# Kernel optimization log

Hardware: AMD Instinct MI355X
Metric: run time of the kernel (lower is better)

The kernel has to match this reference:

```python
import jax, jax.numpy as jnp
import numpy as np

N_EMB = 1024
N_HEADS = 16
HS = N_EMB // N_HEADS  # 64
BASE = 10000.0


def _rope_cache(T):
    # theta uses dim = n_emb (as in the source), sliced to hs//2 frequencies
    i = jnp.arange(HS // 2, dtype=jnp.float32)
    theta = BASE ** (-2.0 * i / N_EMB)            # [hs/2]
    pos = jnp.arange(T, dtype=jnp.float32)        # [T]
    ang = pos[:, None] * theta[None, :]           # [T, hs/2]
    return jnp.cos(ang), jnp.sin(ang)


def _apply_rope(x, cos, sin):
    # x: [B, T, nh, hs]; rotate consecutive pairs along hs
    b, t, nh, hs = x.shape
    xr = x.reshape(b, t, nh, hs // 2, 2)
    c = cos[None, :, None, :]
    s = sin[None, :, None, :]
    r0 = xr[..., 0] * c - xr[..., 1] * s
    r1 = xr[..., 1] * c + xr[..., 0] * s
    return jnp.stack([r0, r1], axis=-1).reshape(b, t, nh, hs)


def setup_inputs() -> dict:
    key = jax.random.key(0)
    k1, k2, k3, k4 = jax.random.split(key, 4)
    B, T = 2, 2048
    w_std = 0.02
    x = jax.random.normal(k1, (B, T, N_EMB), jnp.float32)
    Wq = jax.random.normal(k2, (N_EMB, N_EMB), jnp.float32) * w_std
    Wk = jax.random.normal(k3, (N_EMB, N_EMB), jnp.float32) * w_std
    Wv = jax.random.normal(k4, (N_EMB, N_EMB), jnp.float32) * w_std
    return {"x": x, "Wq": Wq, "Wk": Wk, "Wv": Wv}


def reference(x, Wq, Wk, Wv):
    B, T, C = x.shape
    # nn.Linear(bias=False): y = x @ W.T
    q = (x @ Wq.T).reshape(B, T, N_HEADS, HS)
    k = (x @ Wk.T).reshape(B, T, N_HEADS, HS)
    v = (x @ Wv.T).reshape(B, T, N_HEADS, HS)
    cos, sin = _rope_cache(T)
    q = _apply_rope(q, cos, sin)
    k = _apply_rope(k, cos, sin)
    # scale uses C (n_emb), as in the source (not head_size)
    wei = jnp.einsum('bqhd,bkhd->bhqk', q, k) * (C ** -0.5)  # [B, nh, T, T]
    mask = jnp.tril(jnp.ones((T, T), dtype=bool))
    wei = jnp.where(mask[None, None], wei, -jnp.inf)
    wei = jax.nn.softmax(wei, axis=-1)
    # dropout is identity in eval mode
    out = jnp.einsum('bhqk,bkhd->bqhd', wei, v).reshape(B, T, C)
    return out
```

## Files before the change

kernel.cpp:

```cpp
#include <hip/hip_runtime.h>
#include <stdint.h>

typedef unsigned short u16;
typedef __bf16 bf16x8 __attribute__((ext_vector_type(8)));
typedef unsigned short u16x8 __attribute__((ext_vector_type(8)));
typedef float f32x4 __attribute__((ext_vector_type(4)));

#define LOG2E 1.4426950408889634f

typedef const __attribute__((address_space(1))) uint32_t as1_u32;
typedef __attribute__((address_space(3))) uint32_t as3_u32;

__device__ __forceinline__ u16 f2bf(float f) {
  union { float f; uint32_t i; } v; v.f = f;
  uint32_t r = (v.i + 0x7fffu + ((v.i >> 16) & 1u)) >> 16;
  return (u16)r;
}
__device__ __forceinline__ float bf2f(u16 u) {
  union { uint32_t i; float f; } v; v.i = ((uint32_t)u) << 16; return v.f;
}

__device__ __forceinline__ void gld_lds16(const void* g, void* l) {
  as1_u32* gp = (as1_u32*)((uintptr_t)g);
  as3_u32* lp = (as3_u32*)(uint32_t)(uintptr_t)(l);
  __builtin_amdgcn_global_load_lds(gp, lp, 16, 0, 0);
}

__global__ __launch_bounds__(256) void f32_to_bf16(
    const float* __restrict__ x, const float* __restrict__ wq,
    const float* __restrict__ wk, const float* __restrict__ wv,
    u16* __restrict__ xc, u16* __restrict__ wqc,
    u16* __restrict__ wkc, u16* __restrict__ wvc) {
  const int z = blockIdx.y;
  const float* src = z == 0 ? x : (z == 1 ? wq : (z == 2 ? wk : wv));
  u16* dst = z == 0 ? xc : (z == 1 ? wqc : (z == 2 ? wkc : wvc));
  const int n = z == 0 ? (1 << 22) : (1 << 20);

  const int idx = (blockIdx.x * 256 + (int)threadIdx.x) * 8;
  if (idx >= n) return;
  const f32x4 a = *(const f32x4*)&src[idx];
  const f32x4 b = *(const f32x4*)&src[idx + 4];
  u16x8 o;
#pragma unroll
  for (int j = 0; j < 4; j++) { o[j] = f2bf(a[j]); o[j + 4] = f2bf(b[j]); }
  *(u16x8*)&dst[idx] = o;
}

__global__ __launch_bounds__(256) void qkv_gemm(
    const u16* __restrict__ xc, const u16* __restrict__ wqc,
    const u16* __restrict__ wkc, const u16* __restrict__ wvc,
    u16* __restrict__ qo, u16* __restrict__ ko, u16* __restrict__ vt) {
  __shared__ __align__(16) u16 As[128 * 32];
  __shared__ __align__(16) u16 Bs[128 * 32];

  const int tid = threadIdx.x;
  const int lane = tid & 63;
  const int w = tid >> 6;
  const int wm = w >> 1, wn = w & 1;
  const int quad = lane >> 4, m16 = lane & 15;
  const int which = blockIdx.z;

  const u16* __restrict__ Ap;
  const u16* __restrict__ Bp;
  int m0, n0;
  if (which == 2) {
    Ap = wvc; Bp = xc;
    m0 = blockIdx.x * 128;
    n0 = blockIdx.y * 128;
  } else {
    Ap = xc; Bp = which == 0 ? wqc : wkc;
    m0 = blockIdx.y * 128;
    n0 = blockIdx.x * 128;
  }

  const f32x4 z4 = {0.f, 0.f, 0.f, 0.f};
  f32x4 acc[4][4];
#pragma unroll
  for (int i = 0; i < 4; i++)
#pragma unroll
    for (int j = 0; j < 4; j++) acc[i][j] = z4;

  const int rowA = m0 + w * 32 + (lane >> 2);
  const int rowB = n0 + w * 32 + (lane >> 2);
  const int cch = (lane & 3) * 8;

  for (int k0 = 0; k0 < 1024; k0 += 32) {
    __syncthreads();
#pragma unroll
    for (int i = 0; i < 2; i++) {
      gld_lds16(&Ap[(size_t)(rowA + i * 16) * 1024 + k0 + cch],
                &As[(w * 32 + i * 16) * 32]);
      gld_lds16(&Bp[(size_t)(rowB + i * 16) * 1024 + k0 + cch],
                &Bs[(w * 32 + i * 16) * 32]);
    }
    __syncthreads();

    bf16x8 af[4], bfr[4];
#pragma unroll
    for (int t = 0; t < 4; t++) {
      af[t]  = *(const bf16x8*)&As[(wm * 64 + t * 16 + m16) * 32 + quad * 8];
      bfr[t] = *(const bf16x8*)&Bs[(wn * 64 + t * 16 + m16) * 32 + quad * 8];
    }
#pragma unroll
    for (int mt = 0; mt < 4; mt++)
#pragma unroll
      for (int nt = 0; nt < 4; nt++)
        acc[mt][nt] = __builtin_amdgcn_mfma_f32_16x16x32_bf16(
            af[mt], bfr[nt], acc[mt][nt], 0, 0, 0);
  }

  if (which < 2) {
    u16* __restrict__ out = which == 0 ? qo : ko;
#pragma unroll
    for (int mt = 0; mt < 4; mt++) {
      const int row = m0 + wm * 64 + mt * 16 + quad * 4;
#pragma unroll
      for (int nt = 0; nt < 4; nt++) {
        const int n = n0 + wn * 64 + nt * 16 + m16;
        f32x4 a = acc[mt][nt];
#pragma unroll
        for (int r = 0; r < 4; r++)
          out[(size_t)(row + r) * 1024 + n] = f2bf(a[r]);
      }
    }
  } else {
#pragma unroll
    for (int mt = 0; mt < 4; mt++) {
      const int row = m0 + wm * 64 + mt * 16 + quad * 4;
#pragma unroll
      for (int nt = 0; nt < 4; nt++) {
        const int n = n0 + wn * 64 + nt * 16 + m16;
        f32x4 a = acc[mt][nt];
#pragma unroll
        for (int r = 0; r < 4; r++)
          vt[(size_t)(row + r) * 4096 + n] = f2bf(a[r]);
      }
    }
  }
}

__global__ __launch_bounds__(256) void rope_inplace(u16* __restrict__ qb,
                                                    u16* __restrict__ kb) {
  u16* buf = blockIdx.y == 0 ? qb : kb;
  const int p = blockIdx.x * 256 + (int)threadIdx.x;
  const int nidx = p * 2;
  const int row = nidx >> 10;
  const int col = nidx & 1023;
  const int i = (col & 63) >> 1;
  const int t = row & 2047;
  const float theta = exp2f(-(float)i * 0.02595256324130752f);
  const float ang = (float)t * theta;
  float s, c;
  sincosf(ang, &s, &c);
  const float a0 = bf2f(buf[(size_t)row * 1024 + col]);
  const float a1 = bf2f(buf[(size_t)row * 1024 + col + 1]);
  buf[(size_t)row * 1024 + col]     = f2bf(a0 * c - a1 * s);
  buf[(size_t)row * 1024 + col + 1] = f2bf(a1 * c + a0 * s);
}

__global__ __launch_bounds__(256) void flash_attn(
    const u16* __restrict__ qg, const u16* __restrict__ kg,
    const u16* __restrict__ vt, float* __restrict__ out) {
  __shared__ __align__(16) u16 Qs[64 * 72];
  __shared__ __align__(16) u16 Ks[64 * 72];
  __shared__ __align__(16) u16 Vs[64 * 72];
  __shared__ __align__(16) u16 Ps[64 * 72];

  const int tid = threadIdx.x, lane = tid & 63, w = tid >> 6;
  const int quad = lane >> 4, m16 = lane & 15;
  const int h = blockIdx.y, b = blockIdx.z;
  const size_t base = (size_t)b * 2048 * 1024 + (size_t)h * 64;
  const size_t vbase = (size_t)(h * 64) * 4096 + (size_t)b * 2048;
  const float SC = 0.03125f * LOG2E;

  const f32x4 z4 = {0.f, 0.f, 0.f, 0.f};
  const int srow = tid >> 2, sc = (tid & 3) * 16;

  for (int pass = 0; pass < 2; ++pass) {
    const int qt = pass == 0 ? (int)blockIdx.x : 31 - (int)blockIdx.x;
    const int q0 = qt * 64;

    __syncthreads();
    {
      const u16* src = &qg[base + (size_t)(q0 + srow) * 1024 + sc];
      *(u16x8*)&Qs[srow * 72 + sc] = *(const u16x8*)src;
      *(u16x8*)&Qs[srow * 72 + sc + 8] = *(const u16x8*)(src + 8);
    }
    u16x8 kr0, kr1, vr0, vr1;
    {
      const u16* ks = &kg[base + (size_t)srow * 1024 + sc];
      kr0 = *(const u16x8*)ks; kr1 = *(const u16x8*)(ks + 8);
      const u16* vs = &vt[vbase + (size_t)srow * 4096 + sc];
      vr0 = *(const u16x8*)vs; vr1 = *(const u16x8*)(vs + 8);
    }
    __syncthreads();
    const bf16x8 qf0 = *(const bf16x8*)&Qs[(w * 16 + m16) * 72 + quad * 8];
    const bf16x8 qf1 = *(const bf16x8*)&Qs[(w * 16 + m16) * 72 + 32 + quad * 8];

    float l_p[4] = {0.f, 0.f, 0.f, 0.f};
    f32x4 O[4];
#pragma unroll
    for (int d = 0; d < 4; d++) O[d] = z4;

    const int qrow0 = q0 + w * 16 + quad * 4;

    for (int kt = 0; kt <= qt; ++kt) {
      const int k0 = kt * 64;
      if (kt) __syncthreads();
      *(u16x8*)&Ks[srow * 72 + sc] = kr0;
      *(u16x8*)&Ks[srow * 72 + sc + 8] = kr1;
      *(u16x8*)&Vs[srow * 72 + sc] = vr0;
      *(u16x8*)&Vs[srow * 72 + sc + 8] = vr1;
      __syncthreads();
      if (kt < qt) {
        const u16* ks = &kg[base + (size_t)(k0 + 64 + srow) * 1024 + sc];
        kr0 = *(const u16x8*)ks; kr1 = *(const u16x8*)(ks + 8);
        const u16* vs = &vt[vbase + (size_t)srow * 4096 + k0 + 64 + sc];
        vr0 = *(const u16x8*)vs; vr1 = *(const u16x8*)(vs + 8);
      }

      f32x4 S[4];
#pragma unroll
      for (int nt = 0; nt < 4; nt++) {
        const bf16x8 kf0 = *(const bf16x8*)&Ks[(nt * 16 + m16) * 72 + quad * 8];
        const bf16x8 kf1 =
            *(const bf16x8*)&Ks[(nt * 16 + m16) * 72 + 32 + quad * 8];
        S[nt] = __builtin_amdgcn_mfma_f32_16x16x32_bf16(qf0, kf0, z4, 0, 0, 0);
        S[nt] = __builtin_amdgcn_mfma_f32_16x16x32_bf16(qf1, kf1, S[nt], 0, 0, 0);
      }

      const bool diag = (kt == qt);
#pragma unroll
      for (int nt = 0; nt < 4; nt++) {
        const int key = k0 + nt * 16 + m16;
#pragma unroll
        for (int r = 0; r < 4; r++) {
          float p = exp2f(S[nt][r] * SC);
          if (diag && key > qrow0 + r) p = 0.f;
          union { float f; uint32_t i; } u; u.f = p;
          const uint32_t hi = u.i & 0xffff0000u;
          Ps[(w * 16 + quad * 4 + r) * 72 + nt * 16 + m16] = (u16)(hi >> 16);
          union { uint32_t i; float f; } pr; pr.i = hi;
          l_p[r] += pr.f;
        }
      }

      const bf16x8 pf0 = *(const bf16x8*)&Ps[(w * 16 + m16) * 72 + quad * 8];
      const bf16x8 pf1 =
          *(const bf16x8*)&Ps[(w * 16 + m16) * 72 + 32 + quad * 8];
#pragma unroll
      for (int dt = 0; dt < 4; dt++) {
        const bf16x8 vf0 = *(const bf16x8*)&Vs[(dt * 16 + m16) * 72 + quad * 8];
        const bf16x8 vf1 =
            *(const bf16x8*)&Vs[(dt * 16 + m16) * 72 + 32 + quad * 8];
        O[dt] = __builtin_amdgcn_mfma_f32_16x16x32_bf16(pf0, vf0, O[dt], 0, 0, 0);
        O[dt] = __builtin_amdgcn_mfma_f32_16x16x32_bf16(pf1, vf1, O[dt], 0, 0, 0);
      }
    }

#pragma unroll
    for (int off = 1; off < 16; off <<= 1)
#pragma unroll
      for (int r = 0; r < 4; r++) l_p[r] += __shfl_xor(l_p[r], off);
    float inv[4];
#pragma unroll
    for (int r = 0; r < 4; r++) inv[r] = 1.0f / l_p[r];

#pragma unroll
    for (int dt = 0; dt < 4; dt++)
#pragma unroll
      for (int r = 0; r < 4; r++)
        out[base + (size_t)(qrow0 + r) * 1024 + dt * 16 + m16] =
            O[dt][r] * inv[r];
  }
}

extern "C" void kernel_launch(void* const* d_in, const int* in_sizes, int n_in,
                              void* d_out, int out_size, void* d_ws, size_t ws_size,
                              hipStream_t stream) {
  const float* x  = (const float*)d_in[0];
  const float* Wq = (const float*)d_in[1];
  const float* Wk = (const float*)d_in[2];
  const float* Wv = (const float*)d_in[3];
  u16* qb  = (u16*)d_ws;
  u16* kb  = qb  + (size_t)4096 * 1024;
  u16* vtw = kb  + (size_t)4096 * 1024;
  u16* xc  = vtw + (size_t)4096 * 1024;
  u16* wqc = xc  + (size_t)4096 * 1024;
  u16* wkc = wqc + (size_t)1024 * 1024;
  u16* wvc = wkc + (size_t)1024 * 1024;

  f32_to_bf16<<<dim3(2048, 4), 256, 0, stream>>>(x, Wq, Wk, Wv,
                                                 xc, wqc, wkc, wvc);
  qkv_gemm<<<dim3(8, 32, 3), 256, 0, stream>>>(xc, wqc, wkc, wvc,
                                               qb, kb, vtw);
  rope_inplace<<<dim3(8192, 2), 256, 0, stream>>>(qb, kb);
  flash_attn<<<dim3(16, 16, 2), 256, 0, stream>>>(qb, kb, vtw, (float*)d_out);
}
```

Before: 170.2 us.

## Keep softmax probabilities in registers via transposed S MFMA and permlane swaps

Computes S transposed by swapping the MFMA operands, so each lane holds one query column across keys. The probabilities are packed to bf16 with v_cvt_pk_bf16_f32 and rearranged with v_permlane32_swap into the A-operand layout for the PV MFMA. This removes the Ps shared-memory round trip and shrinks the row-sum shuffle reduction. To keep the fragments consistent, the V tile store is interleaved in 4-element chunks, and the sums are redistributed with shuffles at the end. The approach depends on the exact MFMA lane layout being right, which is easy to get wrong.

```diff
diff --git a/kernel.cpp b/kernel.cpp
--- a/kernel.cpp
+++ b/kernel.cpp
@@ -4,7 +4,9 @@
 typedef unsigned short u16;
 typedef __bf16 bf16x8 __attribute__((ext_vector_type(8)));
 typedef unsigned short u16x8 __attribute__((ext_vector_type(8)));
+typedef unsigned short u16x4 __attribute__((ext_vector_type(4)));
 typedef float f32x4 __attribute__((ext_vector_type(4)));
+typedef uint32_t u32v4 __attribute__((ext_vector_type(4)));
 
 #define LOG2E 1.4426950408889634f
 
@@ -164,7 +166,6 @@
   __shared__ __align__(16) u16 Qs[64 * 72];
   __shared__ __align__(16) u16 Ks[64 * 72];
   __shared__ __align__(16) u16 Vs[64 * 72];
-  __shared__ __align__(16) u16 Ps[64 * 72];
 
   const int tid = threadIdx.x, lane = tid & 63, w = tid >> 6;
   const int quad = lane >> 4, m16 = lane & 15;
@@ -197,20 +198,27 @@
     const bf16x8 qf0 = *(const bf16x8*)&Qs[(w * 16 + m16) * 72 + quad * 8];
     const bf16x8 qf1 = *(const bf16x8*)&Qs[(w * 16 + m16) * 72 + 32 + quad * 8];
 
-    float l_p[4] = {0.f, 0.f, 0.f, 0.f};
+    float l_p = 0.f;
     f32x4 O[4];
 #pragma unroll
     for (int d = 0; d < 4; d++) O[d] = z4;
 
     const int qrow0 = q0 + w * 16 + quad * 4;
+    const int qcol  = q0 + w * 16 + m16;
 
     for (int kt = 0; kt <= qt; ++kt) {
       const int k0 = kt * 64;
       if (kt) __syncthreads();
       *(u16x8*)&Ks[srow * 72 + sc] = kr0;
       *(u16x8*)&Ks[srow * 72 + sc + 8] = kr1;
-      *(u16x8*)&Vs[srow * 72 + sc] = vr0;
-      *(u16x8*)&Vs[srow * 72 + sc + 8] = vr1;
+      {
+        const u16x4* v0 = (const u16x4*)&vr0;
+        const u16x4* v1 = (const u16x4*)&vr1;
+        *(u16x4*)&Vs[srow * 72 + sc]      = v0[0];
+        *(u16x4*)&Vs[srow * 72 + sc + 4]  = v1[0];
+        *(u16x4*)&Vs[srow * 72 + sc + 8]  = v0[1];
+        *(u16x4*)&Vs[srow * 72 + sc + 12] = v1[1];
+      }
       __syncthreads();
       if (kt < qt) {
         const u16* ks = &kg[base + (size_t)(k0 + 64 + srow) * 1024 + sc];
@@ -225,46 +233,57 @@
         const bf16x8 kf0 = *(const bf16x8*)&Ks[(nt * 16 + m16) * 72 + quad * 8];
         const bf16x8 kf1 =
             *(const bf16x8*)&Ks[(nt * 16 + m16) * 72 + 32 + quad * 8];
-        S[nt] = __builtin_amdgcn_mfma_f32_16x16x32_bf16(qf0, kf0, z4, 0, 0, 0);
-        S[nt] = __builtin_amdgcn_mfma_f32_16x16x32_bf16(qf1, kf1, S[nt], 0, 0, 0);
+        S[nt] = __builtin_amdgcn_mfma_f32_16x16x32_bf16(kf0, qf0, z4, 0, 0, 0);
+        S[nt] = __builtin_amdgcn_mfma_f32_16x16x32_bf16(kf1, qf1, S[nt], 0, 0, 0);
       }
 
       const bool diag = (kt == qt);
+      uint32_t W[8];
 #pragma unroll
       for (int nt = 0; nt < 4; nt++) {
-        const int key = k0 + nt * 16 + m16;
+        float p[4];
 #pragma unroll
         for (int r = 0; r < 4; r++) {
-          float p = exp2f(S[nt][r] * SC);
-          if (diag && key > qrow0 + r) p = 0.f;
-          union { float f; uint32_t i; } u; u.f = p;
-          const uint32_t hi = u.i & 0xffff0000u;
-          Ps[(w * 16 + quad * 4 + r) * 72 + nt * 16 + m16] = (u16)(hi >> 16);
-          union { uint32_t i; float f; } pr; pr.i = hi;
-          l_p[r] += pr.f;
+          float e = exp2f(S[nt][r] * SC);
+          const int key = k0 + nt * 16 + quad * 4 + r;
+          if (diag && key > qcol) e = 0.f;
+          p[r] = e;
         }
-      }
-
-      const bf16x8 pf0 = *(const bf16x8*)&Ps[(w * 16 + m16) * 72 + quad * 8];
-      const bf16x8 pf1 =
-          *(const bf16x8*)&Ps[(w * 16 + m16) * 72 + 32 + quad * 8];
+        uint32_t w0, w1;
+        asm("v_cvt_pk_bf16_f32 %0, %1, %2" : "=v"(w0) : "v"(p[0]), "v"(p[1]));
+        asm("v_cvt_pk_bf16_f32 %0, %1, %2" : "=v"(w1) : "v"(p[2]), "v"(p[3]));
+        W[2 * nt] = w0; W[2 * nt + 1] = w1;
+        union { uint32_t i; float f; } e0, e1, e2, e3;
+        e0.i = w0 << 16; e1.i = w0 & 0xffff0000u;
+        e2.i = w1 << 16; e3.i = w1 & 0xffff0000u;
+        l_p += (e0.f + e1.f) + (e2.f + e3.f);
+      }
+
+      uint32_t a0 = W[0], b0 = W[2], a1 = W[1], b1 = W[3];
+      asm("v_permlane32_swap_b32 %0, %1" : "+v"(a0), "+v"(b0));
+      asm("v_permlane32_swap_b32 %0, %1" : "+v"(a1), "+v"(b1));
+      uint32_t a2 = W[4], b2 = W[6], a3 = W[5], b3 = W[7];
+      asm("v_permlane32_swap_b32 %0, %1" : "+v"(a2), "+v"(b2));
+      asm("v_permlane32_swap_b32 %0, %1" : "+v"(a3), "+v"(b3));
+      union { u32v4 u; bf16x8 f; } P0, P1;
+      P0.u = (u32v4){a0, a1, b0, b1};
+      P1.u = (u32v4){a2, a3, b2, b3};
+
 #pragma unroll
       for (int dt = 0; dt < 4; dt++) {
         const bf16x8 vf0 = *(const bf16x8*)&Vs[(dt * 16 + m16) * 72 + quad * 8];
         const bf16x8 vf1 =
             *(const bf16x8*)&Vs[(dt * 16 + m16) * 72 + 32 + quad * 8];
-        O[dt] = __builtin_amdgcn_mfma_f32_16x16x32_bf16(pf0, vf0, O[dt], 0, 0, 0);
-        O[dt] = __builtin_amdgcn_mfma_f32_16x16x32_bf16(pf1, vf1, O[dt], 0, 0, 0);
-      }
-    }
-
-#pragma unroll
-    for (int off = 1; off < 16; off <<= 1)
-#pragma unroll
-      for (int r = 0; r < 4; r++) l_p[r] += __shfl_xor(l_p[r], off);
+        O[dt] = __builtin_amdgcn_mfma_f32_16x16x32_bf16(P0.f, vf0, O[dt], 0, 0, 0);
+        O[dt] = __builtin_amdgcn_mfma_f32_16x16x32_bf16(P1.f, vf1, O[dt], 0, 0, 0);
+      }
+    }
+
+    l_p += __shfl_xor(l_p, 16);
+    l_p += __shfl_xor(l_p, 32);
     float inv[4];
 #pragma unroll
-    for (int r = 0; r < 4; r++) inv[r] = 1.0f / l_p[r];
+    for (int r = 0; r < 4; r++) inv[r] = 1.0f / __shfl(l_p, quad * 4 + r);
 
 #pragma unroll
     for (int dt = 0; dt < 4; dt++)
```

After: 167.7 us. No clear change (-1.4%).
